# Kernel tuning notes

Hardware: AMD Instinct MI355X
Metric: run time of the kernel (lower is better)

## Reference

```python
import jax, jax.numpy as jnp
import numpy as np

THRESHOLD = 1.0


def heaviside(x):
    return (x > 0).astype(x.dtype)


def lif_parallel(x, W_ih, b_ih, b_hh, beta):
    """snntorch LeakyParallel: RNN with relu nonlinearity and diagonal
    recurrent weight = beta, followed by threshold spike (no reset).
    x: [T, B, I]; W_ih: [H, I]; beta: [H]. Returns spikes [T, B, H]."""
    beta = jnp.clip(beta, 0.0, 1.0)
    # input projection is time-parallel (one big GEMM)
    z = jnp.einsum('tbi,hi->tbh', x, W_ih) + b_ih + b_hh  # [T, B, H]

    def step(h, z_t):
        h_new = jax.nn.relu(z_t + beta * h)
        return h_new, h_new

    h0 = jnp.zeros(z.shape[1:], z.dtype)
    _, mem = jax.lax.scan(step, h0, z)  # [T, B, H]
    return heaviside(mem - THRESHOLD)


def setup_inputs() -> dict:
    key = jax.random.key(0)
    ks = jax.random.split(key, 9)
    T, B, I, H, O = 200, 256, 784, 1000, 10
    s1 = 1.0 / np.sqrt(I)
    s2 = 1.0 / np.sqrt(H)
    return {
        'x': jax.random.normal(ks[0], (T, B, I), dtype=jnp.float32),
        'W_ih1': jax.random.normal(ks[1], (H, I), dtype=jnp.float32) * s1,
        'b_ih1': jax.random.normal(ks[2], (H,), dtype=jnp.float32) * s1,
        'b_hh1': jax.random.normal(ks[3], (H,), dtype=jnp.float32) * s1,
        'beta1': jnp.full((H,), 0.95, dtype=jnp.float32),
        'W_ih2': jax.random.normal(ks[4], (O, H), dtype=jnp.float32) * s2,
        'b_ih2': jax.random.normal(ks[5], (O,), dtype=jnp.float32) * s2,
        'b_hh2': jax.random.normal(ks[6], (O,), dtype=jnp.float32) * s2,
        'beta2': jnp.full((O,), 0.95, dtype=jnp.float32),
    }


def reference(x, W_ih1, b_ih1, b_hh1, beta1, W_ih2, b_ih2, b_hh2, beta2):
    spk1 = lif_parallel(x, W_ih1, b_ih1, b_hh1, beta1)   # [T, B, 1000]
    spk2 = lif_parallel(spk1, W_ih2, b_ih2, b_hh2, beta2)  # [T, B, 10]
    return spk2
```

## Files before the change

kernel.cpp:

```cpp
#include <hip/hip_runtime.h>
#include <cstdint>
#include <cstddef>

#define T_STEPS 200
#define B_SZ    256
#define I_SZ    784
#define H_SZ    1000
#define O_SZ    10
#define M_ROWS  (T_STEPS * B_SZ)

#define GBM 128
#define GBN 128
#define GBK 32
#define LDW 132

__device__ __forceinline__ int swz(int g) {
    return (g & 24) | ((g + (g >> 3)) & 7);
}

__global__ __launch_bounds__(256, 4) void gemm1_fp32_v2(
    const float* __restrict__ X, const float* __restrict__ W,
    const float* __restrict__ b_ih, const float* __restrict__ b_hh,
    float* __restrict__ Z)
{
    __shared__ float As[GBK * LDW];
    __shared__ float Bs[GBK * LDW];

    const int tid  = threadIdx.x;
    const int tr   = tid >> 4;
    const int tc   = tid & 15;
    const int row0 = blockIdx.x * GBM;
    const int col0 = blockIdx.y * GBN;

    const int a0 = swz(2 * tr)     * 4;
    const int a1 = swz(2 * tr + 1) * 4;
    const int b0 = swz(2 * tc)     * 4;
    const int b1 = swz(2 * tc + 1) * 4;

    float acc[8][8] = {};

    const float* Xp = X + (size_t)row0 * I_SZ;
    const float* Wp = W + (size_t)col0 * I_SZ;

    for (int k0 = 0; k0 < I_SZ; k0 += GBK) {
        #pragma unroll
        for (int l = 0; l < 4; ++l) {
            int id = tid + l * 256;
            int r  = id >> 3;
            int c4 = id & 7;
            int k  = k0 + c4 * 4;
            int base = swz(r >> 2) * 4 + (r & 3);

            float4 av = make_float4(0.f, 0.f, 0.f, 0.f);
            if (k + 4 <= I_SZ)
                av = *(const float4*)(Xp + (size_t)r * I_SZ + k);
            As[(4*c4 + 0) * LDW + base] = av.x;
            As[(4*c4 + 1) * LDW + base] = av.y;
            As[(4*c4 + 2) * LDW + base] = av.z;
            As[(4*c4 + 3) * LDW + base] = av.w;

            float4 bv = make_float4(0.f, 0.f, 0.f, 0.f);
            if (k + 4 <= I_SZ && col0 + r < H_SZ)
                bv = *(const float4*)(Wp + (size_t)r * I_SZ + k);
            Bs[(4*c4 + 0) * LDW + base] = bv.x;
            Bs[(4*c4 + 1) * LDW + base] = bv.y;
            Bs[(4*c4 + 2) * LDW + base] = bv.z;
            Bs[(4*c4 + 3) * LDW + base] = bv.w;
        }
        __syncthreads();

        #pragma unroll 4
        for (int k = 0; k < GBK; ++k) {
            const int kb = k * LDW;
            float4 A0 = *(const float4*)&As[kb + a0];
            float4 A1 = *(const float4*)&As[kb + a1];
            float4 B0 = *(const float4*)&Bs[kb + b0];
            float4 B1 = *(const float4*)&Bs[kb + b1];
            float a[8] = {A0.x, A0.y, A0.z, A0.w, A1.x, A1.y, A1.z, A1.w};
            float b[8] = {B0.x, B0.y, B0.z, B0.w, B1.x, B1.y, B1.z, B1.w};
            #pragma unroll
            for (int i = 0; i < 8; ++i)
                #pragma unroll
                for (int j = 0; j < 8; ++j)
                    acc[i][j] = fmaf(a[i], b[j], acc[i][j]);
        }
        __syncthreads();
    }

    float bias[8];
    #pragma unroll
    for (int j = 0; j < 8; ++j) {
        int cc = col0 + tc * 8 + j;
        bias[j] = (cc < H_SZ) ? (b_ih[cc] + b_hh[cc]) : 0.f;
    }

    const bool full = (col0 + 127 < H_SZ);
    #pragma unroll
    for (int i = 0; i < 8; ++i) {
        int rr = row0 + tr * 8 + i;
        float* zrow = Z + (size_t)rr * H_SZ + col0 + tc * 8;
        if (full) {
            float4 v0 = make_float4(acc[i][0] + bias[0], acc[i][1] + bias[1],
                                    acc[i][2] + bias[2], acc[i][3] + bias[3]);
            float4 v1 = make_float4(acc[i][4] + bias[4], acc[i][5] + bias[5],
                                    acc[i][6] + bias[6], acc[i][7] + bias[7]);
            *(float4*)(zrow + 0) = v0;
            *(float4*)(zrow + 4) = v1;
        } else {
            #pragma unroll
            for (int j = 0; j < 8; ++j) {
                int cc = col0 + tc * 8 + j;
                if (cc < H_SZ) zrow[j] = acc[i][j] + bias[j];
            }
        }
    }
}

__global__ __launch_bounds__(256) void scan1_kernel(
    float* __restrict__ Z, const float* __restrict__ beta)
{
    int idx = blockIdx.x * blockDim.x + threadIdx.x;
    if (idx >= B_SZ * H_SZ) return;
    int h = idx % H_SZ;
    float be = fminf(fmaxf(beta[h], 0.f), 1.f);
    float hm = 0.f;
    const size_t stride = (size_t)B_SZ * H_SZ;
    float* p = Z + idx;
    for (int t = 0; t < T_STEPS; ++t) {
        float v = p[(size_t)t * stride];
        hm = fmaxf(fmaf(be, hm, v), 0.f);
        p[(size_t)t * stride] = (hm > 1.0f) ? 1.0f : 0.0f;
    }
}

__global__ __launch_bounds__(256) void gemm2_kernel(
    const float* __restrict__ S, const float* __restrict__ W2,
    const float* __restrict__ b_ih2, const float* __restrict__ b_hh2,
    float* __restrict__ Z2)
{
    __shared__ float W2s[O_SZ * H_SZ];
    for (int i = threadIdx.x; i < O_SZ * H_SZ; i += blockDim.x)
        W2s[i] = W2[i];
    __syncthreads();

    const int wave  = threadIdx.x >> 6;
    const int lane  = threadIdx.x & 63;
    const int wgid  = blockIdx.x * (blockDim.x >> 6) + wave;
    const int nwave = gridDim.x * (blockDim.x >> 6);

    for (int m = wgid; m < M_ROWS; m += nwave) {
        const float* row = S + (size_t)m * H_SZ;
        float acc[O_SZ];
        #pragma unroll
        for (int o = 0; o < O_SZ; ++o) acc[o] = 0.f;

        for (int h = lane; h < H_SZ; h += 64) {
            float s = row[h];
            #pragma unroll
            for (int o = 0; o < O_SZ; ++o)
                acc[o] = fmaf(s, W2s[o * H_SZ + h], acc[o]);
        }
        #pragma unroll
        for (int o = 0; o < O_SZ; ++o) {
            float v = acc[o];
            #pragma unroll
            for (int off = 32; off > 0; off >>= 1)
                v += __shfl_down(v, off, 64);
            if (lane == 0)
                Z2[(size_t)m * O_SZ + o] = v + b_ih2[o] + b_hh2[o];
        }
    }
}

#define CH 20
__global__ __launch_bounds__(256) void scan2_kernel(
    const float* __restrict__ Z2, const float* __restrict__ beta2,
    float* __restrict__ out)
{
    int idx = blockIdx.x * blockDim.x + threadIdx.x;
    if (idx >= B_SZ * O_SZ) return;
    int o = idx % O_SZ;
    float be = fminf(fmaxf(beta2[o], 0.f), 1.f);
    float hm = 0.f;
    const int stride = B_SZ * O_SZ;
    for (int t0 = 0; t0 < T_STEPS; t0 += CH) {
        float v[CH];
        #pragma unroll
        for (int i = 0; i < CH; ++i)
            v[i] = Z2[(size_t)(t0 + i) * stride + idx];
        #pragma unroll
        for (int i = 0; i < CH; ++i) {
            hm = fmaxf(fmaf(be, hm, v[i]), 0.f);
            out[(size_t)(t0 + i) * stride + idx] = (hm > 1.0f) ? 1.0f : 0.0f;
        }
    }
}

extern "C" void kernel_launch(void* const* d_in, const int* in_sizes, int n_in,
                              void* d_out, int out_size, void* d_ws, size_t ws_size,
                              hipStream_t stream)
{
    const float* x     = (const float*)d_in[0];
    const float* W1    = (const float*)d_in[1];
    const float* bih1  = (const float*)d_in[2];
    const float* bhh1  = (const float*)d_in[3];
    const float* beta1 = (const float*)d_in[4];
    const float* W2    = (const float*)d_in[5];
    const float* bih2  = (const float*)d_in[6];
    const float* bhh2  = (const float*)d_in[7];
    const float* beta2 = (const float*)d_in[8];
    float* out = (float*)d_out;

    float* z1 = (float*)d_ws;
    float* z2 = z1 + (size_t)M_ROWS * H_SZ;

    dim3 g1(M_ROWS / GBM, (H_SZ + GBN - 1) / GBN);
    gemm1_fp32_v2<<<g1, 256, 0, stream>>>(x, W1, bih1, bhh1, z1);

    scan1_kernel<<<(B_SZ * H_SZ) / 256, 256, 0, stream>>>(z1, beta1);
    gemm2_kernel<<<2048, 256, 0, stream>>>(z1, W2, bih2, bhh2, z2);
    scan2_kernel<<<(B_SZ * O_SZ + 255) / 256, 256, 0, stream>>>(z2, beta2, out);
}
```

Measured before the change: 1.203 ms.

## Pre-pack GEMM1 operands into swizzled tiles and load via direct global-to-LDS

Adds a pack kernel that rearranges X and W1 into K-major, swizzled 128x32 tiles in workspace. GEMM1 can then fill LDS with contiguous 16-byte global_load_lds transfers instead of scalar transposing stores. The block index is also remapped to group blocks by N-tile for L2 reuse, and layer-2 output is written in place to the output buffer, which removes the z2 workspace. In exchange, packing adds extra passes over X (about 160MB read plus write), and the GEMM still has no double buffering.

```diff
diff --git a/kernel.cpp b/kernel.cpp
--- a/kernel.cpp
+++ b/kernel.cpp
@@ -9,73 +9,107 @@
 #define O_SZ    10
 #define M_ROWS  (T_STEPS * B_SZ)
 
-#define GBM 128
-#define GBN 128
-#define GBK 32
-#define LDW 132
-
-__device__ __forceinline__ int swz(int g) {
-    return (g & 24) | ((g + (g >> 3)) & 7);
-}
-
-__global__ __launch_bounds__(256, 4) void gemm1_fp32_v2(
-    const float* __restrict__ X, const float* __restrict__ W,
+#define KT        25
+#define TILE_WORDS 4096
+#define MBLKS     400
+#define NBLKS     8
+
+__device__ __forceinline__ int swz32(int g) { return (g & 24) | ((g + (g >> 3)) & 7); }
+__device__ __forceinline__ int inv32(int p) { return (p & 24) | ((p - (p >> 3)) & 7); }
+
+typedef const __attribute__((address_space(1))) void gvoid;
+typedef __attribute__((address_space(3))) void lvoid;
+__device__ __forceinline__ void gload16(const void* g, void* l) {
+    __builtin_amdgcn_global_load_lds((gvoid*)g, (lvoid*)l, 16, 0, 0);
+}
+
+__global__ __launch_bounds__(256) void pack_kernel(
+    const float* __restrict__ src, float* __restrict__ dst, int nrows)
+{
+    int bid = blockIdx.x;
+    int blk = bid / KT, kt = bid - blk * KT;
+
+    __shared__ float T[32 * 132];
+    const int tid = threadIdx.x;
+
+    #pragma unroll
+    for (int it = 0; it < 4; ++it) {
+        int id = tid + it * 256;
+        int r  = id >> 3;
+        int c4 = id & 7;
+        int row = blk * 128 + r;
+        int k   = kt * 32 + c4 * 4;
+        float4 v = make_float4(0.f, 0.f, 0.f, 0.f);
+        if (row < nrows && k < I_SZ)
+            v = *(const float4*)(src + (size_t)row * I_SZ + k);
+        T[(c4*4 + 0) * 132 + r] = v.x;
+        T[(c4*4 + 1) * 132 + r] = v.y;
+        T[(c4*4 + 2) * 132 + r] = v.z;
+        T[(c4*4 + 3) * 132 + r] = v.w;
+    }
+    __syncthreads();
+
+    float* out = dst + (size_t)(blk * KT + kt) * TILE_WORDS;
+    #pragma unroll
+    for (int it = 0; it < 4; ++it) {
+        int id = tid + it * 256;
+        int k  = id >> 5;
+        int pg = id & 31;
+        int g  = inv32(pg);
+        float4 v = *(const float4*)&T[k * 132 + g * 4];
+        *(float4*)(out + k * 128 + pg * 4) = v;
+    }
+}
+
+__global__ __launch_bounds__(256, 4) void gemm1_v3(
+    const float* __restrict__ Xp, const float* __restrict__ Wp,
     const float* __restrict__ b_ih, const float* __restrict__ b_hh,
     float* __restrict__ Z)
 {
-    __shared__ float As[GBK * LDW];
-    __shared__ float Bs[GBK * LDW];
-
-    const int tid  = threadIdx.x;
-    const int tr   = tid >> 4;
-    const int tc   = tid & 15;
-    const int row0 = blockIdx.x * GBM;
-    const int col0 = blockIdx.y * GBN;
-
-    const int a0 = swz(2 * tr)     * 4;
-    const int a1 = swz(2 * tr + 1) * 4;
-    const int b0 = swz(2 * tc)     * 4;
-    const int b1 = swz(2 * tc + 1) * 4;
+    __shared__ float Al[TILE_WORDS];
+    __shared__ float Bl[TILE_WORDS];
+
+    const int tid = threadIdx.x;
+    const int tr  = tid >> 4;
+    const int tc  = tid & 15;
+
+    int bid  = blockIdx.x;
+    int wg   = (bid & 7) * 400 + (bid >> 3);
+    int mblk = wg >> 3;
+    int nblk = wg & 7;
+    const int row0 = mblk * 128;
+    const int col0 = nblk * 128;
+
+    const int a0 = swz32(2*tr)     * 4;
+    const int a1 = swz32(2*tr + 1) * 4;
+    const int b0 = swz32(2*tc)     * 4;
+    const int b1 = swz32(2*tc + 1) * 4;
+
+    const float* pA = Xp + (size_t)mblk * KT * TILE_WORDS;
+    const float* pB = Wp + (size_t)nblk * KT * TILE_WORDS;
 
     float acc[8][8] = {};
 
-    const float* Xp = X + (size_t)row0 * I_SZ;
-    const float* Wp = W + (size_t)col0 * I_SZ;
-
-    for (int k0 = 0; k0 < I_SZ; k0 += GBK) {
-        #pragma unroll
-        for (int l = 0; l < 4; ++l) {
-            int id = tid + l * 256;
-            int r  = id >> 3;
-            int c4 = id & 7;
-            int k  = k0 + c4 * 4;
-            int base = swz(r >> 2) * 4 + (r & 3);
-
-            float4 av = make_float4(0.f, 0.f, 0.f, 0.f);
-            if (k + 4 <= I_SZ)
-                av = *(const float4*)(Xp + (size_t)r * I_SZ + k);
-            As[(4*c4 + 0) * LDW + base] = av.x;
-            As[(4*c4 + 1) * LDW + base] = av.y;
-            As[(4*c4 + 2) * LDW + base] = av.z;
-            As[(4*c4 + 3) * LDW + base] = av.w;
-
-            float4 bv = make_float4(0.f, 0.f, 0.f, 0.f);
-            if (k + 4 <= I_SZ && col0 + r < H_SZ)
-                bv = *(const float4*)(Wp + (size_t)r * I_SZ + k);
-            Bs[(4*c4 + 0) * LDW + base] = bv.x;
-            Bs[(4*c4 + 1) * LDW + base] = bv.y;
-            Bs[(4*c4 + 2) * LDW + base] = bv.z;
-            Bs[(4*c4 + 3) * LDW + base] = bv.w;
-        }
+    for (int kt = 0; kt < KT; ++kt) {
+        const float* sA = pA + kt * TILE_WORDS + tid * 4;
+        const float* sB = pB + kt * TILE_WORDS + tid * 4;
+        gload16(sA,        &Al[        tid * 4]);
+        gload16(sA + 1024, &Al[1024 + tid * 4]);
+        gload16(sA + 2048, &Al[2048 + tid * 4]);
+        gload16(sA + 3072, &Al[3072 + tid * 4]);
+        gload16(sB,        &Bl[        tid * 4]);
+        gload16(sB + 1024, &Bl[1024 + tid * 4]);
+        gload16(sB + 2048, &Bl[2048 + tid * 4]);
+        gload16(sB + 3072, &Bl[3072 + tid * 4]);
         __syncthreads();
 
-        #pragma unroll 4
-        for (int k = 0; k < GBK; ++k) {
-            const int kb = k * LDW;
-            float4 A0 = *(const float4*)&As[kb + a0];
-            float4 A1 = *(const float4*)&As[kb + a1];
-            float4 B0 = *(const float4*)&Bs[kb + b0];
-            float4 B1 = *(const float4*)&Bs[kb + b1];
+        #pragma unroll 2
+        for (int k = 0; k < 32; ++k) {
+            const int kb = k * 128;
+            float4 A0 = *(const float4*)&Al[kb + a0];
+            float4 A1 = *(const float4*)&Al[kb + a1];
+            float4 B0 = *(const float4*)&Bl[kb + b0];
+            float4 B1 = *(const float4*)&Bl[kb + b1];
             float a[8] = {A0.x, A0.y, A0.z, A0.w, A1.x, A1.y, A1.z, A1.w};
             float b[8] = {B0.x, B0.y, B0.z, B0.w, B1.x, B1.y, B1.z, B1.w};
             #pragma unroll
@@ -174,8 +208,7 @@
 
 #define CH 20
 __global__ __launch_bounds__(256) void scan2_kernel(
-    const float* __restrict__ Z2, const float* __restrict__ beta2,
-    float* __restrict__ out)
+    float* __restrict__ Z2io, const float* __restrict__ beta2)
 {
     int idx = blockIdx.x * blockDim.x + threadIdx.x;
     if (idx >= B_SZ * O_SZ) return;
@@ -187,11 +220,11 @@
         float v[CH];
         #pragma unroll
         for (int i = 0; i < CH; ++i)
-            v[i] = Z2[(size_t)(t0 + i) * stride + idx];
+            v[i] = Z2io[(size_t)(t0 + i) * stride + idx];
         #pragma unroll
         for (int i = 0; i < CH; ++i) {
             hm = fmaxf(fmaf(be, hm, v[i]), 0.f);
-            out[(size_t)(t0 + i) * stride + idx] = (hm > 1.0f) ? 1.0f : 0.0f;
+            Z2io[(size_t)(t0 + i) * stride + idx] = (hm > 1.0f) ? 1.0f : 0.0f;
         }
     }
 }
@@ -211,13 +244,17 @@
     const float* beta2 = (const float*)d_in[8];
     float* out = (float*)d_out;
 
-    float* z1 = (float*)d_ws;
-    float* z2 = z1 + (size_t)M_ROWS * H_SZ;
-
-    dim3 g1(M_ROWS / GBM, (H_SZ + GBN - 1) / GBN);
-    gemm1_fp32_v2<<<g1, 256, 0, stream>>>(x, W1, bih1, bhh1, z1);
+    char* base = (char*)d_ws;
+    float* z1 = (float*)base;
+    float* Xp = (float*)(base + (size_t)M_ROWS * H_SZ * 4);
+    float* Wp = Xp + (size_t)MBLKS * KT * TILE_WORDS;
+
+    pack_kernel<<<MBLKS * KT, 256, 0, stream>>>(x,  Xp, M_ROWS);
+    pack_kernel<<<NBLKS * KT, 256, 0, stream>>>(W1, Wp, H_SZ);
+
+    gemm1_v3<<<MBLKS * NBLKS, 256, 0, stream>>>(Xp, Wp, bih1, bhh1, z1);
 
     scan1_kernel<<<(B_SZ * H_SZ) / 256, 256, 0, stream>>>(z1, beta1);
-    gemm2_kernel<<<2048, 256, 0, stream>>>(z1, W2, bih2, bhh2, z2);
-    scan2_kernel<<<(B_SZ * O_SZ + 255) / 256, 256, 0, stream>>>(z2, beta2, out);
-}
+    gemm2_kernel<<<2048, 256, 0, stream>>>(z1, W2, bih2, bhh2, out);
+    scan2_kernel<<<(B_SZ * O_SZ + 255) / 256, 256, 0, stream>>>(out, beta2);
+}
```

Result: no change. 1.184 ms (-1.6%).
